# Kernel optimization log

Measured on AMD Instinct MI355X. Metric: run time of the kernel, lower is better.

Reference implementation:

```python
import jax, jax.numpy as jnp
import numpy as np

B, T, I, H = 4, 512, 128, 128


def _lstm(x, Wih, Whh, b):
    """Standard LSTM (PyTorch gate order i,f,g,o). x: [B,T,I] -> h: [B,T,H]."""
    xg = jnp.swapaxes(x, 0, 1) @ Wih.T + b  # [T,B,4H] input projections precomputed
    Hh = Whh.shape[1]
    h0 = jnp.zeros((x.shape[0], Hh), x.dtype)
    c0 = jnp.zeros((x.shape[0], Hh), x.dtype)

    def step(carry, xg_t):
        h, c = carry
        g = xg_t + h @ Whh.T
        i, f, gg, o = jnp.split(g, 4, axis=-1)
        c = jax.nn.sigmoid(f) * c + jax.nn.sigmoid(i) * jnp.tanh(gg)
        h = jax.nn.sigmoid(o) * jnp.tanh(c)
        return (h, c), h

    _, hs = jax.lax.scan(step, (h0, c0), xg)
    return jnp.swapaxes(hs, 0, 1)  # [B,T,H]


def setup_inputs() -> dict:
    key = jax.random.key(0)
    ks = jax.random.split(key, 12)
    s = 0.1
    return {
        "x": jax.random.normal(ks[0], (B, T, I), jnp.float32),
        # shared LSTM
        "Wih_s": jax.random.normal(ks[1], (4 * H, I), jnp.float32) * s,
        "Whh_s": jax.random.normal(ks[2], (4 * H, H), jnp.float32) * s,
        "b_lstm_s": jnp.zeros((4 * H,), jnp.float32),
        # Ws split along its concatenated input [x_sub; h_t; h_sub]
        "Wx": jax.random.normal(ks[3], (I, H), jnp.float32) * s,
        "Wht": jax.random.normal(ks[4], (H, H), jnp.float32) * s,
        "Whs": jax.random.normal(ks[5], (H, H), jnp.float32) * s,
        "bs": jnp.zeros((H,), jnp.float32),
        # Us: H -> 1
        "u": jax.random.normal(ks[6], (H,), jnp.float32) * s,
        "bu": jnp.zeros((), jnp.float32),
        # task LSTM over [x; R] (input_size + hidden_size)
        "Wih_t": jax.random.normal(ks[7], (4 * H, I + H), jnp.float32) * s,
        "Whh_t": jax.random.normal(ks[8], (4 * H, H), jnp.float32) * s,
        "b_lstm_t": jnp.zeros((4 * H,), jnp.float32),
    }


def reference(x, Wih_s, Whh_s, b_lstm_s, Wx, Wht, Whs, bs, u, bu,
              Wih_t, Whh_t, b_lstm_t):
    # 1) shared LSTM encoding
    Hsh = _lstm(x, Wih_s, Whh_s, b_lstm_s)  # [B,T,H]

    # 2) pairwise attention scores S[b,t,s] = Us(tanh(Ws([x_s; h_t; h_s])))
    #    decompose Ws over its concatenated input to avoid building the concat
    xp = x @ Wx          # [B,T,H] (indexed by s)
    hp_t = Hsh @ Wht     # [B,T,H] (indexed by t)
    hp_s = Hsh @ Whs     # [B,T,H] (indexed by s)
    # M[b,t,s,:]: [B,T,T,H] — the dominant (memory-bound) intermediate
    M = jnp.tanh(hp_t[:, :, None, :] + (xp + hp_s)[:, None, :, :] + bs)
    scores = jnp.einsum("btsh,h->bts", M, u) + bu  # [B,T,T]

    # 3) softmax over sub_t and weighted sum of shared outputs
    beta = jax.nn.softmax(scores, axis=-1)         # [B,T,T]
    R = jnp.einsum("bts,bsh->bth", beta, Hsh)      # [B,T,H]

    # 4) task-specific LSTM consuming the input and the aggregated message
    h_task = _lstm(jnp.concatenate([x, R], axis=-1), Wih_t, Whh_t, b_lstm_t)
    return h_task  # [B,T,H]
```

## Files before the change

### kernel.cpp

```cpp
#include <hip/hip_runtime.h>
#include <hip/hip_bf16.h>
#include <math.h>

#define Bq 4
#define Tq 512
#define Hq 128

typedef _Float16 f16x4 __attribute__((ext_vector_type(4)));
typedef _Float16 f16x8 __attribute__((ext_vector_type(8)));
typedef float f32x4 __attribute__((ext_vector_type(4)));

__device__ __forceinline__ float rcp_fast(float x) { return __builtin_amdgcn_rcpf(x); }
__device__ __forceinline__ float sigmoid_fast(float x) {
    return rcp_fast(1.0f + __expf(-x));
}
__device__ __forceinline__ float tanh_fast(float x) {
    float e = __expf(2.0f * x);
    return 1.0f - 2.0f * rcp_fast(e + 1.0f);
}

__device__ __forceinline__ void gemm_nt_body(float (*As)[68], float (*Ws)[68],
                                             const float* __restrict__ A, int lda,
                                             const float* __restrict__ W, int ldw,
                                             const float* __restrict__ bias,
                                             float* __restrict__ C, int acc_flag,
                                             int m0, int n0, int tid) {
    int tx = tid & 15, ty = tid >> 4;
    float acc[4][4] = {};
    for (int kc = 0; kc < 2; kc++) {
        __syncthreads();
#pragma unroll
        for (int i = 0; i < 4; i++) {
            int idx = tid + 256 * i;
            int r = idx >> 4, c4 = idx & 15;
            *(float4*)(&As[r][c4 * 4]) = *(const float4*)(A + (size_t)(m0 + r) * lda + kc * 64 + c4 * 4);
            *(float4*)(&Ws[r][c4 * 4]) = *(const float4*)(W + (size_t)(n0 + r) * ldw + kc * 64 + c4 * 4);
        }
        __syncthreads();
#pragma unroll
        for (int k4 = 0; k4 < 16; k4++) {
            float4 a[4], wv[4];
#pragma unroll
            for (int i = 0; i < 4; i++) a[i] = *(const float4*)(&As[ty * 4 + i][k4 * 4]);
#pragma unroll
            for (int j = 0; j < 4; j++) wv[j] = *(const float4*)(&Ws[tx * 4 + j][k4 * 4]);
#pragma unroll
            for (int i = 0; i < 4; i++)
#pragma unroll
                for (int j = 0; j < 4; j++)
                    acc[i][j] += a[i].x * wv[j].x + a[i].y * wv[j].y + a[i].z * wv[j].z + a[i].w * wv[j].w;
        }
    }
#pragma unroll
    for (int i = 0; i < 4; i++) {
        int m = m0 + ty * 4 + i;
        int n = n0 + tx * 4;
        float4 v = make_float4(acc[i][0], acc[i][1], acc[i][2], acc[i][3]);
        if (bias) { v.x += bias[n]; v.y += bias[n + 1]; v.z += bias[n + 2]; v.w += bias[n + 3]; }
        if (acc_flag) {
            float4 o = *(const float4*)(C + (size_t)m * 512 + n);
            v.x += o.x; v.y += o.y; v.z += o.z; v.w += o.w;
        }
        *(float4*)(C + (size_t)m * 512 + n) = v;
    }
}

__global__ __launch_bounds__(256) void prep(const float* __restrict__ x,
                                            const float* __restrict__ Wih_s,
                                            const float* __restrict__ b_s,
                                            const float* __restrict__ Wih_t,
                                            const float* __restrict__ b_t,
                                            const float* __restrict__ Whh_s,
                                            const float* __restrict__ Whh_t,
                                            float* __restrict__ xg_s,
                                            float* __restrict__ xg_t,
                                            _Float16* __restrict__ W16_s,
                                            _Float16* __restrict__ W16_t) {
    __shared__ __align__(16) float As[64][68];
    __shared__ __align__(16) float Ws[64][68];
    int bid = blockIdx.x;
    int tid = threadIdx.x;
    if (bid < 512) {
        int which = bid >> 8;
        int b2 = bid & 255;
        int m0 = (b2 & 31) * 64, n0 = (b2 >> 5) * 64;
        gemm_nt_body(As, Ws, x, 128,
                     which ? Wih_t : Wih_s, which ? 256 : 128,
                     which ? b_t : b_s,
                     which ? xg_t : xg_s, 0, m0, n0, tid);
    } else {
        int cb = bid - 512;
        const float* in = (cb < 64) ? Whh_s : Whh_t;
        _Float16* out = (cb < 64) ? W16_s : W16_t;
        int i = ((cb & 63) * 256 + tid) * 4;
        float4 v = *(const float4*)(in + i);
        f16x4 o;
        o[0] = (_Float16)v.x; o[1] = (_Float16)v.y;
        o[2] = (_Float16)v.z; o[3] = (_Float16)v.w;
        *(f16x4*)(out + i) = o;
    }
}

__global__ __launch_bounds__(256) void gemm_nt(const float* __restrict__ A, int lda,
                                               const float* __restrict__ W, int ldw,
                                               const float* __restrict__ bias,
                                               float* __restrict__ C, int acc_flag) {
    __shared__ __align__(16) float As[64][68];
    __shared__ __align__(16) float Ws[64][68];
    gemm_nt_body(As, Ws, A, lda, W, ldw, bias, C, acc_flag,
                 blockIdx.x * 64, blockIdx.y * 64, threadIdx.x);
}

__global__ __launch_bounds__(256) void mid(const float* __restrict__ x,
                                           const float* __restrict__ Hsh,
                                           const float* __restrict__ Wht,
                                           const float* __restrict__ Wx,
                                           const float* __restrict__ Whs,
                                           const float* __restrict__ bs,
                                           float* __restrict__ hp_t,
                                           float* __restrict__ c_s) {
    __shared__ __align__(16) float As[64][68];
    __shared__ __align__(16) float Bs[64][68];
    int bid = blockIdx.x;
    int cfg = bid >> 6;
    int b2 = bid & 63;
    int m0 = (b2 & 31) * 64, n0 = (b2 >> 5) * 64;
    const float* A1 = cfg ? x : Hsh;
    const float* B1 = cfg ? Wx : Wht;
    const float* A2 = cfg ? Hsh : nullptr;
    const float* B2 = cfg ? Whs : nullptr;
    const float* bias = cfg ? bs : nullptr;
    float* C = cfg ? c_s : hp_t;

    int tid = threadIdx.x;
    int tx = tid & 15, ty = tid >> 4;
    float acc[4][4] = {};
    for (int src = 0; src < 2; src++) {
        const float* A = src ? A2 : A1;
        const float* Bm = src ? B2 : B1;
        if (!A) break;
        for (int kc = 0; kc < 2; kc++) {
            __syncthreads();
#pragma unroll
            for (int i = 0; i < 4; i++) {
                int idx = tid + 256 * i;
                int r = idx >> 4, c4 = idx & 15;
                *(float4*)(&As[r][c4 * 4]) = *(const float4*)(A + (size_t)(m0 + r) * 128 + kc * 64 + c4 * 4);
                *(float4*)(&Bs[r][c4 * 4]) = *(const float4*)(Bm + (size_t)(kc * 64 + r) * 128 + n0 + c4 * 4);
            }
            __syncthreads();
#pragma unroll
            for (int k4 = 0; k4 < 16; k4++) {
                float4 a[4];
#pragma unroll
                for (int i = 0; i < 4; i++) a[i] = *(const float4*)(&As[ty * 4 + i][k4 * 4]);
#pragma unroll
                for (int kk = 0; kk < 4; kk++) {
                    float4 bv = *(const float4*)(&Bs[k4 * 4 + kk][tx * 4]);
#pragma unroll
                    for (int i = 0; i < 4; i++) {
                        float av = (kk == 0) ? a[i].x : (kk == 1) ? a[i].y : (kk == 2) ? a[i].z : a[i].w;
                        acc[i][0] += av * bv.x;
                        acc[i][1] += av * bv.y;
                        acc[i][2] += av * bv.z;
                        acc[i][3] += av * bv.w;
                    }
                }
            }
        }
    }
#pragma unroll
    for (int i = 0; i < 4; i++) {
        int m = m0 + ty * 4 + i;
        int n = n0 + tx * 4;
        float4 v = make_float4(acc[i][0], acc[i][1], acc[i][2], acc[i][3]);
        if (bias) { v.x += bias[n]; v.y += bias[n + 1]; v.z += bias[n + 2]; v.w += bias[n + 3]; }
        *(float4*)(C + (size_t)m * 128 + n) = v;
    }
}

#define MF0(ACC, A, B) \
    asm("v_mfma_f32_16x16x32_f16 %0, %1, %2, %3" : "=&v"(ACC) : "v"(A), "a"(B), "v"(zro));
#define MF(ACC, A, B) \
    asm("v_mfma_f32_16x16x32_f16 %0, %1, %2, %0" : "+v"(ACC) : "v"(A), "a"(B));

#define LSTM_STEP(X0, X1, X2, X3, R0, R1, R2, R3, WPTR, PXG)                       \
    {                                                                              \
        f16x8 a0 = *(R0); f16x8 a1 = *(R1);                                        \
        f16x8 a2 = *(R2); f16x8 a3 = *(R3);                                        \
        float o0 = X0, o1 = X1, o2 = X2, o3 = X3;                                  \
        X0 = (PXG)[0]; X1 = (PXG)[128]; X2 = (PXG)[256]; X3 = (PXG)[384];          \
        (PXG) += 1024;                                                             \
        f32x4 ac0a, ac1a, ac2a, ac3a, ac0b, ac1b, ac2b, ac3b;                      \
        MF0(ac0a, a0, b00) MF0(ac1a, a0, b10) MF0(ac2a, a0, b20) MF0(ac3a, a0, b30)\
        MF0(ac0b, a2, b02) MF0(ac1b, a2, b12) MF0(ac2b, a2, b22) MF0(ac3b, a2, b32)\
        MF(ac0a, a1, b01) MF(ac1a, a1, b11) MF(ac2a, a1, b21) MF(ac3a, a1, b31)    \
        MF(ac0b, a3, b03) MF(ac1b, a3, b13) MF(ac2b, a3, b23) MF(ac3b, a3, b33)    \
        asm volatile("s_nop 7\n\ts_nop 7"                                          \
                     : "+v"(ac0a), "+v"(ac1a), "+v"(ac2a), "+v"(ac3a),             \
                       "+v"(ac0b), "+v"(ac1b), "+v"(ac2b), "+v"(ac3b));            \
        float gi = ac0a[0] + ac0b[0] + o0;                                         \
        float gf = ac1a[0] + ac1b[0] + o1;                                         \
        float gg = ac2a[0] + ac2b[0] + o2;                                         \
        float go = ac3a[0] + ac3b[0] + o3;                                         \
        float si = sigmoid_fast(gi), sf = sigmoid_fast(gf), so = sigmoid_fast(go); \
        float tg = tanh_fast(gg);                                                  \
        c = sf * c + si * tg;                                                      \
        float h = so * tanh_fast(c);                                               \
        *(WPTR) = (_Float16)h;                                                     \
        *pH = h; pH += Hq;                                                         \
        __builtin_amdgcn_sched_barrier(0);                                         \
        asm volatile("s_waitcnt lgkmcnt(0)");                                      \
        __builtin_amdgcn_s_barrier();                                              \
        __builtin_amdgcn_sched_barrier(0);                                         \
    }

__global__ __launch_bounds__(512)
__attribute__((amdgpu_waves_per_eu(2, 2)))
void lstm_b4(const float* __restrict__ xg,
             const _Float16* __restrict__ W16,
             float* __restrict__ Hout) {
    int tid = threadIdx.x;
    int w = tid >> 6, lane = tid & 63;
    int r = lane & 15, kg = lane >> 4;
    int ch = 16 * w + r;

    __shared__ _Float16 hbuf[2][16][128];
    _Float16* hbase = &hbuf[0][0][0];
    for (int i = tid; i < 4096; i += 512) hbase[i] = (_Float16)0.f;

    const _Float16* wb = W16 + (size_t)ch * 128 + kg * 8;
#define LWB(g, kb) *(const f16x8*)(wb + (size_t)(g) * 16384 + (kb) * 32)
    f16x8 b00 = LWB(0, 0), b01 = LWB(0, 1), b02 = LWB(0, 2), b03 = LWB(0, 3);
    f16x8 b10 = LWB(1, 0), b11 = LWB(1, 1), b12 = LWB(1, 2), b13 = LWB(1, 3);
    f16x8 b20 = LWB(2, 0), b21 = LWB(2, 1), b22 = LWB(2, 2), b23 = LWB(2, 3);
    f16x8 b30 = LWB(3, 0), b31 = LWB(3, 1), b32 = LWB(3, 2), b33 = LWB(3, 3);
#undef LWB
    f32x4 zro = {0.f, 0.f, 0.f, 0.f};
    asm volatile(""
                 : "+a"(b00), "+a"(b01), "+a"(b02), "+a"(b03),
                   "+a"(b10), "+a"(b11), "+a"(b12), "+a"(b13),
                   "+a"(b20), "+a"(b21), "+a"(b22), "+a"(b23),
                   "+a"(b30), "+a"(b31), "+a"(b32), "+a"(b33),
                   "+v"(zro));

    int aoff0 = r * 128 + (((0 * 4 + kg) ^ r) << 3);
    int aoff1 = r * 128 + (((1 * 4 + kg) ^ r) << 3);
    int aoff2 = r * 128 + (((2 * 4 + kg) ^ r) << 3);
    int aoff3 = r * 128 + (((3 * 4 + kg) ^ r) << 3);
    int woff = (4 * kg) * 128 + (((ch >> 3) ^ (4 * kg)) << 3) + (ch & 7);

    const f16x8* rA0 = (const f16x8*)(hbase + aoff0);
    const f16x8* rA1 = (const f16x8*)(hbase + aoff1);
    const f16x8* rA2 = (const f16x8*)(hbase + aoff2);
    const f16x8* rA3 = (const f16x8*)(hbase + aoff3);
    const f16x8* rB0 = (const f16x8*)(hbase + 2048 + aoff0);
    const f16x8* rB1 = (const f16x8*)(hbase + 2048 + aoff1);
    const f16x8* rB2 = (const f16x8*)(hbase + 2048 + aoff2);
    const f16x8* rB3 = (const f16x8*)(hbase + 2048 + aoff3);
    _Float16* wA = hbase + 2048 + woff;
    _Float16* wB = hbase + woff;

    size_t kgTq = (size_t)kg * Tq;
    const float* xgb = xg;
    const float* p0 = xgb + (kgTq + 0) * 512 + ch;
    const float* p1 = xgb + (kgTq + 1) * 512 + ch;
    float xa0 = p0[0], xa1 = p0[128], xa2 = p0[256], xa3 = p0[384];
    float xb0 = p1[0], xb1 = p1[128], xb2 = p1[256], xb3 = p1[384];
    const float* pA = xgb + (kgTq + 2) * 512 + ch;
    const float* pB = xgb + (kgTq + 3) * 512 + ch;
    float* pH = Hout + kgTq * Hq + ch;

    float c = 0.f;
    __syncthreads();

    for (int t = 0; t < Tq; t += 2) {
        LSTM_STEP(xa0, xa1, xa2, xa3, rA0, rA1, rA2, rA3, wA, pA)
        LSTM_STEP(xb0, xb1, xb2, xb3, rB0, rB1, rB2, rB3, wB, pB)
    }
}

__global__ __launch_bounds__(256) void attn_kernel(const float* __restrict__ hp_t,
                                                   const float* __restrict__ c_s,
                                                   const float* __restrict__ u,
                                                   const float* __restrict__ Hsh,
                                                   float* __restrict__ R) {
    int t = blockIdx.x, b = blockIdx.y;
    int tid = threadIdx.x;
    __shared__ __align__(16) float a_lds[128];
    __shared__ __align__(16) float u_lds[128];
    __shared__ __align__(16) float sc[512];
    __shared__ __align__(16) float red[256];

    if (tid < 128) {
        a_lds[tid] = hp_t[((size_t)b * Tq + t) * Hq + tid];
        u_lds[tid] = u[tid];
    }
    __syncthreads();

    int lane = tid & 63, wv = tid >> 6;
    int h4 = lane & 15, s2 = lane >> 4;
    float4 a0 = *(const float4*)(&a_lds[h4 * 4]);
    float4 a1 = *(const float4*)(&a_lds[64 + h4 * 4]);
    float4 u0 = *(const float4*)(&u_lds[h4 * 4]);
    float4 u1 = *(const float4*)(&u_lds[64 + h4 * 4]);

    const float* cb = c_s + (size_t)b * Tq * Hq;
    float psum = 0.0f;
#pragma unroll 4
    for (int it = 0; it < 32; ++it) {
        int s = it * 16 + wv * 4 + s2;
        const float4* crow = (const float4*)(cb + (size_t)s * Hq);
        float4 c0 = crow[h4];
        float4 c1 = crow[h4 + 16];
        float acc = u0.x * tanh_fast(a0.x + c0.x) + u0.y * tanh_fast(a0.y + c0.y)
                  + u0.z * tanh_fast(a0.z + c0.z) + u0.w * tanh_fast(a0.w + c0.w)
                  + u1.x * tanh_fast(a1.x + c1.x) + u1.y * tanh_fast(a1.y + c1.y)
                  + u1.z * tanh_fast(a1.z + c1.z) + u1.w * tanh_fast(a1.w + c1.w);
        acc += __shfl_xor(acc, 1, 64);
        acc += __shfl_xor(acc, 2, 64);
        acc += __shfl_xor(acc, 4, 64);
        acc += __shfl_xor(acc, 8, 64);
        if (h4 == 0) {
            float p = __expf(acc);
            sc[s] = p;
            psum += p;
        }
    }
#pragma unroll
    for (int off = 1; off < 64; off <<= 1) psum += __shfl_xor(psum, off, 64);
    if (lane == 0) red[wv] = psum;
    __syncthreads();
    float rinv = rcp_fast(red[0] + red[1] + red[2] + red[3]);

    int h = tid & 127, half = tid >> 7;
    float acc = 0.0f;
    for (int s = half; s < 512; s += 2) {
        acc += sc[s] * Hsh[((size_t)b * Tq + s) * Hq + h];
    }
    red[tid] = acc;
    __syncthreads();
    if (tid < 128) {
        R[((size_t)b * Tq + t) * Hq + tid] = (red[tid] + red[tid + 128]) * rinv;
    }
}

extern "C" void kernel_launch(void* const* d_in, const int* in_sizes, int n_in,
                              void* d_out, int out_size, void* d_ws, size_t ws_size,
                              hipStream_t stream) {
    const float* x      = (const float*)d_in[0];
    const float* Wih_s  = (const float*)d_in[1];
    const float* Whh_s  = (const float*)d_in[2];
    const float* b_s    = (const float*)d_in[3];
    const float* Wx     = (const float*)d_in[4];
    const float* Wht    = (const float*)d_in[5];
    const float* Whs    = (const float*)d_in[6];
    const float* bs     = (const float*)d_in[7];
    const float* u      = (const float*)d_in[8];
    const float* Wih_t  = (const float*)d_in[10];
    const float* Whh_t  = (const float*)d_in[11];
    const float* b_t    = (const float*)d_in[12];
    float* out = (float*)d_out;

    float* ws    = (float*)d_ws;
    float* xg_s  = ws;
    float* xg_t  = ws + 1048576;
    float* Hsh   = ws + 2097152;
    float* hp_t  = ws + 2359296;
    float* c_s   = ws + 2621440;
    float* Rbuf  = ws + 2883584;
    _Float16* W16_t = (_Float16*)(ws + 3145728);
    _Float16* W16_s = (_Float16*)hp_t;

    dim3 blk(256);

    prep<<<640, blk, 0, stream>>>(x, Wih_s, b_s, Wih_t, b_t, Whh_s, Whh_t,
                                  xg_s, xg_t, W16_s, W16_t);

    lstm_b4<<<1, 512, 0, stream>>>(xg_s, W16_s, Hsh);

    mid<<<128, blk, 0, stream>>>(x, Hsh, Wht, Wx, Whs, bs, hp_t, c_s);

    attn_kernel<<<dim3(Tq, Bq), blk, 0, stream>>>(hp_t, c_s, u, Hsh, Rbuf);

    gemm_nt<<<dim3(32, 8), blk, 0, stream>>>(Rbuf, 128, Wih_t + 128, 256, nullptr, xg_t, 1);

    lstm_b4<<<1, 512, 0, stream>>>(xg_t, W16_t, out);
}
```

Measured before the change: 636.4 us.

## Process eight query rows per attention block to reuse key loads

The attention kernel now handles 8 consecutive t rows per block, one 32-lane group per row. Each c_s and Hsh row load is shared across those rows, and the per-row max-free softmax sum is kept per thread. This cuts global and L2 traffic for the keys and values in exchange for fewer blocks. Each thread also gets a long serial loop over all 512 keys with a 5-step shuffle reduction, and the exp is computed redundantly in every lane.

```diff
diff --git a/kernel.cpp b/kernel.cpp
--- a/kernel.cpp
+++ b/kernel.cpp
@@ -285,64 +285,61 @@
                                                    const float* __restrict__ u,
                                                    const float* __restrict__ Hsh,
                                                    float* __restrict__ R) {
-    int t = blockIdx.x, b = blockIdx.y;
+    int t0 = blockIdx.x * 8;
+    int b = blockIdx.y;
     int tid = threadIdx.x;
-    __shared__ __align__(16) float a_lds[128];
-    __shared__ __align__(16) float u_lds[128];
-    __shared__ __align__(16) float sc[512];
-    __shared__ __align__(16) float red[256];
-
-    if (tid < 128) {
-        a_lds[tid] = hp_t[((size_t)b * Tq + t) * Hq + tid];
-        u_lds[tid] = u[tid];
+    int h8 = tid & 31;
+    int tq = tid >> 5;
+
+    __shared__ __align__(16) float a_lds[8][128];
+    __shared__ __align__(16) float sc[8][512];
+
+    {
+        int idx = tid * 4;
+        int row = idx >> 7, col = idx & 127;
+        *(float4*)&a_lds[row][col] =
+            *(const float4*)(hp_t + ((size_t)b * Tq + t0 + row) * Hq + col);
     }
     __syncthreads();
 
-    int lane = tid & 63, wv = tid >> 6;
-    int h4 = lane & 15, s2 = lane >> 4;
-    float4 a0 = *(const float4*)(&a_lds[h4 * 4]);
-    float4 a1 = *(const float4*)(&a_lds[64 + h4 * 4]);
-    float4 u0 = *(const float4*)(&u_lds[h4 * 4]);
-    float4 u1 = *(const float4*)(&u_lds[64 + h4 * 4]);
-
-    const float* cb = c_s + (size_t)b * Tq * Hq;
-    float psum = 0.0f;
+    float4 av = *(const float4*)&a_lds[tq][h8 * 4];
+    float4 uv = *(const float4*)(u + h8 * 4);
+
+    const float* cb = c_s + (size_t)b * Tq * Hq + h8 * 4;
+    float dsum = 0.f;
 #pragma unroll 4
-    for (int it = 0; it < 32; ++it) {
-        int s = it * 16 + wv * 4 + s2;
-        const float4* crow = (const float4*)(cb + (size_t)s * Hq);
-        float4 c0 = crow[h4];
-        float4 c1 = crow[h4 + 16];
-        float acc = u0.x * tanh_fast(a0.x + c0.x) + u0.y * tanh_fast(a0.y + c0.y)
-                  + u0.z * tanh_fast(a0.z + c0.z) + u0.w * tanh_fast(a0.w + c0.w)
-                  + u1.x * tanh_fast(a1.x + c1.x) + u1.y * tanh_fast(a1.y + c1.y)
-                  + u1.z * tanh_fast(a1.z + c1.z) + u1.w * tanh_fast(a1.w + c1.w);
+    for (int s = 0; s < 512; ++s) {
+        float4 cv = *(const float4*)(cb + (size_t)s * Hq);
+        float acc = uv.x * tanh_fast(av.x + cv.x) + uv.y * tanh_fast(av.y + cv.y)
+                  + uv.z * tanh_fast(av.z + cv.z) + uv.w * tanh_fast(av.w + cv.w);
         acc += __shfl_xor(acc, 1, 64);
         acc += __shfl_xor(acc, 2, 64);
         acc += __shfl_xor(acc, 4, 64);
         acc += __shfl_xor(acc, 8, 64);
-        if (h4 == 0) {
-            float p = __expf(acc);
-            sc[s] = p;
-            psum += p;
-        }
-    }
-#pragma unroll
-    for (int off = 1; off < 64; off <<= 1) psum += __shfl_xor(psum, off, 64);
-    if (lane == 0) red[wv] = psum;
+        acc += __shfl_xor(acc, 16, 64);
+        float p = __expf(acc);
+        if (h8 == 0) sc[tq][s] = p;
+        dsum += p;
+    }
+    float rinv = rcp_fast(dsum);
     __syncthreads();
-    float rinv = rcp_fast(red[0] + red[1] + red[2] + red[3]);
-
-    int h = tid & 127, half = tid >> 7;
-    float acc = 0.0f;
-    for (int s = half; s < 512; s += 2) {
-        acc += sc[s] * Hsh[((size_t)b * Tq + s) * Hq + h];
-    }
-    red[tid] = acc;
-    __syncthreads();
-    if (tid < 128) {
-        R[((size_t)b * Tq + t) * Hq + tid] = (red[tid] + red[tid + 128]) * rinv;
-    }
+
+    const float* hb = Hsh + (size_t)b * Tq * Hq + h8 * 4;
+    float ax = 0.f, ay = 0.f, az = 0.f, aw = 0.f;
+#pragma unroll 2
+    for (int s4 = 0; s4 < 512; s4 += 4) {
+        float4 w4 = *(const float4*)&sc[tq][s4];
+        float4 v0 = *(const float4*)(hb + (size_t)(s4 + 0) * Hq);
+        float4 v1 = *(const float4*)(hb + (size_t)(s4 + 1) * Hq);
+        float4 v2 = *(const float4*)(hb + (size_t)(s4 + 2) * Hq);
+        float4 v3 = *(const float4*)(hb + (size_t)(s4 + 3) * Hq);
+        ax += w4.x * v0.x + w4.y * v1.x + w4.z * v2.x + w4.w * v3.x;
+        ay += w4.x * v0.y + w4.y * v1.y + w4.z * v2.y + w4.w * v3.y;
+        az += w4.x * v0.z + w4.y * v1.z + w4.z * v2.z + w4.w * v3.z;
+        aw += w4.x * v0.w + w4.y * v1.w + w4.z * v2.w + w4.w * v3.w;
+    }
+    float4 outv = make_float4(ax * rinv, ay * rinv, az * rinv, aw * rinv);
+    *(float4*)(R + ((size_t)b * Tq + t0 + tq) * Hq + h8 * 4) = outv;
 }
 
 extern "C" void kernel_launch(void* const* d_in, const int* in_sizes, int n_in,
@@ -381,7 +378,7 @@
 
     mid<<<128, blk, 0, stream>>>(x, Hsh, Wht, Wx, Whs, bs, hp_t, c_s);
 
-    attn_kernel<<<dim3(Tq, Bq), blk, 0, stream>>>(hp_t, c_s, u, Hsh, Rbuf);
+    attn_kernel<<<dim3(Tq / 8, Bq), blk, 0, stream>>>(hp_t, c_s, u, Hsh, Rbuf);
 
     gemm_nt<<<dim3(32, 8), blk, 0, stream>>>(Rbuf, 128, Wih_t + 128, 256, nullptr, xg_t, 1);
 
```

After: 801.8 us. 1.26x slower.

## Overlap task-LSTM input projection and weight cast with the shared LSTM

Applied to the files above, without the earlier changes.

The x-part of the task LSTM input projection and the fp16 cast of Whh_t move out of the prep kernel into a fused launch. Block 0 of that launch runs the sequential shared LSTM while the other blocks compute the projection and the cast on otherwise idle CUs. This shortens the prep kernel that sits ahead of the latency-bound recurrence, and it adds a 512-thread GEMM variant plus a shared LDS buffer. The risk is that the concurrent blocks compete with the LSTM block for memory bandwidth or for its CU.

```diff
diff --git a/kernel.cpp b/kernel.cpp
--- a/kernel.cpp
+++ b/kernel.cpp
@@ -65,39 +65,69 @@
     }
 }
 
+__device__ __forceinline__ void gemm_nt_512(float (*As)[68], float (*Ws)[68],
+                                            const float* __restrict__ A, int lda,
+                                            const float* __restrict__ W, int ldw,
+                                            const float* __restrict__ bias,
+                                            float* __restrict__ C,
+                                            int m0, int n0, int tid) {
+    int tx = tid & 15, ty = tid >> 4;
+    float acc[2][4] = {};
+    for (int kc = 0; kc < 2; kc++) {
+        __syncthreads();
+#pragma unroll
+        for (int i = 0; i < 2; i++) {
+            int idx = tid + 512 * i;
+            int r = idx >> 4, c4 = idx & 15;
+            *(float4*)(&As[r][c4 * 4]) = *(const float4*)(A + (size_t)(m0 + r) * lda + kc * 64 + c4 * 4);
+            *(float4*)(&Ws[r][c4 * 4]) = *(const float4*)(W + (size_t)(n0 + r) * ldw + kc * 64 + c4 * 4);
+        }
+        __syncthreads();
+#pragma unroll
+        for (int k4 = 0; k4 < 16; k4++) {
+            float4 a[2], wv[4];
+#pragma unroll
+            for (int i = 0; i < 2; i++) a[i] = *(const float4*)(&As[ty * 2 + i][k4 * 4]);
+#pragma unroll
+            for (int j = 0; j < 4; j++) wv[j] = *(const float4*)(&Ws[tx * 4 + j][k4 * 4]);
+#pragma unroll
+            for (int i = 0; i < 2; i++)
+#pragma unroll
+                for (int j = 0; j < 4; j++)
+                    acc[i][j] += a[i].x * wv[j].x + a[i].y * wv[j].y + a[i].z * wv[j].z + a[i].w * wv[j].w;
+        }
+    }
+#pragma unroll
+    for (int i = 0; i < 2; i++) {
+        int m = m0 + ty * 2 + i;
+        int n = n0 + tx * 4;
+        float4 v = make_float4(acc[i][0], acc[i][1], acc[i][2], acc[i][3]);
+        if (bias) { v.x += bias[n]; v.y += bias[n + 1]; v.z += bias[n + 2]; v.w += bias[n + 3]; }
+        *(float4*)(C + (size_t)m * 512 + n) = v;
+    }
+}
+
 __global__ __launch_bounds__(256) void prep(const float* __restrict__ x,
                                             const float* __restrict__ Wih_s,
                                             const float* __restrict__ b_s,
-                                            const float* __restrict__ Wih_t,
-                                            const float* __restrict__ b_t,
                                             const float* __restrict__ Whh_s,
-                                            const float* __restrict__ Whh_t,
                                             float* __restrict__ xg_s,
-                                            float* __restrict__ xg_t,
-                                            _Float16* __restrict__ W16_s,
-                                            _Float16* __restrict__ W16_t) {
+                                            _Float16* __restrict__ W16_s) {
     __shared__ __align__(16) float As[64][68];
     __shared__ __align__(16) float Ws[64][68];
     int bid = blockIdx.x;
     int tid = threadIdx.x;
-    if (bid < 512) {
-        int which = bid >> 8;
-        int b2 = bid & 255;
-        int m0 = (b2 & 31) * 64, n0 = (b2 >> 5) * 64;
-        gemm_nt_body(As, Ws, x, 128,
-                     which ? Wih_t : Wih_s, which ? 256 : 128,
-                     which ? b_t : b_s,
-                     which ? xg_t : xg_s, 0, m0, n0, tid);
+    if (bid < 256) {
+        gemm_nt_body(As, Ws, x, 128, Wih_s, 128, b_s, xg_s, 0,
+                     (bid & 31) * 64, (bid >> 5) * 64, tid);
     } else {
-        int cb = bid - 512;
-        const float* in = (cb < 64) ? Whh_s : Whh_t;
-        _Float16* out = (cb < 64) ? W16_s : W16_t;
-        int i = ((cb & 63) * 256 + tid) * 4;
-        float4 v = *(const float4*)(in + i);
+        int cb = bid - 256;
+        int i = (cb * 256 + tid) * 4;
+        float4 v = *(const float4*)(Whh_s + i);
         f16x4 o;
         o[0] = (_Float16)v.x; o[1] = (_Float16)v.y;
         o[2] = (_Float16)v.z; o[3] = (_Float16)v.w;
-        *(f16x4*)(out + i) = o;
+        *(f16x4*)(W16_s + i) = o;
     }
 }
 
@@ -215,18 +245,14 @@
         __builtin_amdgcn_sched_barrier(0);                                         \
     }
 
-__global__ __launch_bounds__(512)
-__attribute__((amdgpu_waves_per_eu(2, 2)))
-void lstm_b4(const float* __restrict__ xg,
-             const _Float16* __restrict__ W16,
-             float* __restrict__ Hout) {
-    int tid = threadIdx.x;
+__device__ __forceinline__ void lstm_core(const float* __restrict__ xg,
+                                          const _Float16* __restrict__ W16,
+                                          float* __restrict__ Hout,
+                                          _Float16* hbase, int tid) {
     int w = tid >> 6, lane = tid & 63;
     int r = lane & 15, kg = lane >> 4;
     int ch = 16 * w + r;
 
-    __shared__ _Float16 hbuf[2][16][128];
-    _Float16* hbase = &hbuf[0][0][0];
     for (int i = tid; i < 4096; i += 512) hbase[i] = (_Float16)0.f;
 
     const _Float16* wb = W16 + (size_t)ch * 128 + kg * 8;
@@ -262,13 +288,12 @@
     _Float16* wB = hbase + woff;
 
     size_t kgTq = (size_t)kg * Tq;
-    const float* xgb = xg;
-    const float* p0 = xgb + (kgTq + 0) * 512 + ch;
-    const float* p1 = xgb + (kgTq + 1) * 512 + ch;
+    const float* p0 = xg + (kgTq + 0) * 512 + ch;
+    const float* p1 = xg + (kgTq + 1) * 512 + ch;
     float xa0 = p0[0], xa1 = p0[128], xa2 = p0[256], xa3 = p0[384];
     float xb0 = p1[0], xb1 = p1[128], xb2 = p1[256], xb3 = p1[384];
-    const float* pA = xgb + (kgTq + 2) * 512 + ch;
-    const float* pB = xgb + (kgTq + 3) * 512 + ch;
+    const float* pA = xg + (kgTq + 2) * 512 + ch;
+    const float* pB = xg + (kgTq + 3) * 512 + ch;
     float* pH = Hout + kgTq * Hq + ch;
 
     float c = 0.f;
@@ -278,6 +303,44 @@
         LSTM_STEP(xa0, xa1, xa2, xa3, rA0, rA1, rA2, rA3, wA, pA)
         LSTM_STEP(xb0, xb1, xb2, xb3, rB0, rB1, rB2, rB3, wB, pB)
     }
+}
+
+__global__ __launch_bounds__(512)
+__attribute__((amdgpu_waves_per_eu(2, 2)))
+void lstm_fused(const float* __restrict__ xg_s,
+                const _Float16* __restrict__ W16_s,
+                float* __restrict__ Hsh,
+                const float* __restrict__ x,
+                const float* __restrict__ Wih_t,
+                const float* __restrict__ b_t,
+                const float* __restrict__ Whh_t,
+                float* __restrict__ xg_t,
+                _Float16* __restrict__ W16_t) {
+    __shared__ __align__(16) float smem[2][64][68];
+    int bid = blockIdx.x;
+    int tid = threadIdx.x;
+    if (bid == 0) {
+        lstm_core(xg_s, W16_s, Hsh, (_Float16*)&smem[0][0][0], tid);
+    } else if (bid <= 256) {
+        int b2 = bid - 1;
+        gemm_nt_512(smem[0], smem[1], x, 128, Wih_t, 256, b_t, xg_t,
+                    (b2 & 31) * 64, (b2 >> 5) * 64, tid);
+    } else {
+        int cb = bid - 257;
+        int i = (cb * 512 + tid) * 2;
+        float2 v = *(const float2*)(Whh_t + i);
+        W16_t[i] = (_Float16)v.x;
+        W16_t[i + 1] = (_Float16)v.y;
+    }
+}
+
+__global__ __launch_bounds__(512)
+__attribute__((amdgpu_waves_per_eu(2, 2)))
+void lstm_b4(const float* __restrict__ xg,
+             const _Float16* __restrict__ W16,
+             float* __restrict__ Hout) {
+    __shared__ _Float16 hbuf[2][16][128];
+    lstm_core(xg, W16, Hout, &hbuf[0][0][0], threadIdx.x);
 }
 
 __global__ __launch_bounds__(256) void attn_kernel(const float* __restrict__ hp_t,
@@ -374,10 +437,10 @@
 
     dim3 blk(256);
 
-    prep<<<640, blk, 0, stream>>>(x, Wih_s, b_s, Wih_t, b_t, Whh_s, Whh_t,
-                                  xg_s, xg_t, W16_s, W16_t);
-
-    lstm_b4<<<1, 512, 0, stream>>>(xg_s, W16_s, Hsh);
+    prep<<<320, blk, 0, stream>>>(x, Wih_s, b_s, Whh_s, xg_s, W16_s);
+
+    lstm_fused<<<321, 512, 0, stream>>>(xg_s, W16_s, Hsh,
+                                        x, Wih_t, b_t, Whh_t, xg_t, W16_t);
 
     mid<<<128, blk, 0, stream>>>(x, Hsh, Wht, Wx, Whs, bs, hp_t, c_s);
 
```

New measurement: 624.9 us. No clear change (-1.8%).
